# Performance work log

Hardware: AMD Instinct MI355X
Metric: run time of the kernel (lower is better)

Reference implementation:

```python
import jax, jax.numpy as jnp
import numpy as np

B, S, HID = 2, 2048, 2048
H, HKV, D = 16, 8, 128
CHUNK = 512
THETA = 1000000.0
NEG = -1e9


def setup_inputs() -> dict:
    key = jax.random.key(0)
    ks = jax.random.split(key, 10)
    hidden_states = jax.random.normal(ks[0], (B, S, HID), dtype=jnp.float32)
    # additive causal mask (0 on/below diagonal, -1e9 above)
    tri = jnp.tril(jnp.ones((S, S), dtype=bool))
    attention_mask = jnp.where(tri, 0.0, NEG).astype(jnp.float32)
    attention_mask = jnp.broadcast_to(attention_mask[None, None], (B, 1, S, S))
    w = 0.02
    Wq = jax.random.normal(ks[1], (HID, H * D), dtype=jnp.float32) * w
    bq = jax.random.normal(ks[2], (H * D,), dtype=jnp.float32) * w
    Wk = jax.random.normal(ks[3], (HID, HKV * D), dtype=jnp.float32) * w
    bk = jax.random.normal(ks[4], (HKV * D,), dtype=jnp.float32) * w
    Wv = jax.random.normal(ks[5], (HID, HKV * D), dtype=jnp.float32) * w
    bv = jax.random.normal(ks[6], (HKV * D,), dtype=jnp.float32) * w
    Wo = jax.random.normal(ks[7], (H * D, HID), dtype=jnp.float32) * w
    bo = jax.random.normal(ks[8], (HID,), dtype=jnp.float32) * w
    return {"hidden_states": hidden_states, "attention_mask": attention_mask,
            "Wq": Wq, "bq": bq, "Wk": Wk, "bk": bk, "Wv": Wv, "bv": bv,
            "Wo": Wo, "bo": bo}


def _rope_tables(seq_len, dim):
    inv_freq = 1.0 / (THETA ** (jnp.arange(0, dim, 2, dtype=jnp.float32) / dim))
    pos = jnp.arange(seq_len, dtype=jnp.float32)
    freqs = pos[:, None] * inv_freq[None, :]          # [S, D/2]
    emb = jnp.concatenate([freqs, freqs], axis=-1)    # [S, D]
    return jnp.cos(emb)[None, None], jnp.sin(emb)[None, None]  # [1,1,S,D]


def _rotate_half(x):
    x1, x2 = jnp.split(x, 2, axis=-1)
    return jnp.concatenate([-x2, x1], axis=-1)


def _attn_forward(hidden_states, attention_mask, Wq, bq, Wk, bk, Wv, bv, Wo, bo):
    bsz, s, _ = hidden_states.shape
    q = (hidden_states @ Wq + bq).reshape(bsz, s, H, D).transpose(0, 2, 1, 3)
    k = (hidden_states @ Wk + bk).reshape(bsz, s, HKV, D).transpose(0, 2, 1, 3)
    v = (hidden_states @ Wv + bv).reshape(bsz, s, HKV, D).transpose(0, 2, 1, 3)
    cos, sin = _rope_tables(s, D)
    q = q * cos + _rotate_half(q) * sin
    k = k * cos + _rotate_half(k) * sin
    n_rep = H // HKV
    k = jnp.repeat(k, n_rep, axis=1)  # repeat_kv
    v = jnp.repeat(v, n_rep, axis=1)
    scale = 1.0 / jnp.sqrt(jnp.float32(D))
    nq, nk = s // CHUNK, s // CHUNK
    Qc = q.reshape(bsz, H, nq, CHUNK, D)
    Kc = jnp.moveaxis(k.reshape(bsz, H, nk, CHUNK, D), 2, 0)   # [nk,B,H,Ck,D]
    Vc = jnp.moveaxis(v.reshape(bsz, H, nk, CHUNK, D), 2, 0)
    Mc = jnp.moveaxis(attention_mask.reshape(bsz, 1, nq, CHUNK, nk, CHUNK), 4, 0)  # [nk,B,1,nq,Cq,Ck]

    def step(carry, xs):
        o, m, d = carry
        k_seg, v_seg, m_seg = xs
        # scores: [B,H,nq,Cq,Ck]
        sc = jnp.einsum('bhqcd,bhkd->bhqck', Qc, k_seg) * scale + m_seg
        new_m = jnp.maximum(m, sc.max(axis=-1, keepdims=True))
        e = jnp.exp(sc - new_m)
        sums = e.sum(axis=-1, keepdims=True)
        prev = jnp.exp(m - new_m)          # NOTE: uses running max, as in source
        d_new = prev + sums
        o = (o * prev + jnp.einsum('bhqck,bhkd->bhqcd', e, v_seg)) / d_new
        return (o, new_m, d_new), None

    o0 = jnp.zeros((bsz, H, nq, CHUNK, D), dtype=jnp.float32)
    m0 = jnp.full((bsz, H, nq, CHUNK, 1), -jnp.inf, dtype=jnp.float32)
    d0 = jnp.ones((bsz, H, nq, CHUNK, 1), dtype=jnp.float32)
    (o, m, d), _ = jax.lax.scan(step, (o0, m0, d0), (Kc, Vc, Mc))
    # final rescale: attn_output * exp(max - logsumexp) == o / d_last (source math)
    o = o / d
    attn = o.reshape(bsz, H, s, D).transpose(0, 2, 1, 3).reshape(bsz, s, H * D)
    return attn @ Wo + bo


def reference(hidden_states, attention_mask, Wq, bq, Wk, bk, Wv, bv, Wo, bo):
    return _attn_forward(hidden_states, attention_mask, Wq, bq, Wk, bk, Wv, bv, Wo, bo)
```

## Files before the change

kernel.cpp:

```cpp
#include <hip/hip_runtime.h>
#include <hip/hip_bf16.h>


typedef __attribute__((ext_vector_type(8))) short s8v;
typedef __attribute__((ext_vector_type(4))) float f4v;
typedef __attribute__((ext_vector_type(4))) unsigned int u32x4;

#define MFMA16(a, b, c) __builtin_amdgcn_mfma_f32_16x16x32_bf16((a), (b), (c), 0, 0, 0)

typedef unsigned short u16;
typedef const __attribute__((address_space(1))) unsigned int* gas_p;
typedef __attribute__((address_space(3))) unsigned int* las_p;

template <bool B> struct BoolC { static constexpr bool value = B; };

__device__ __forceinline__ void gl_lds16(const void* g, void* l) {
    __builtin_amdgcn_global_load_lds((gas_p)g, (las_p)l, 16, 0, 0);
}

__device__ __forceinline__ u16 f2b(float f) {
    __hip_bfloat16 h = __float2bfloat16(f);
    return *reinterpret_cast<u16*>(&h);
}
__device__ __forceinline__ float b2f(u16 u) {
    __hip_bfloat16 h;
    *reinterpret_cast<u16*>(&h) = u;
    return __bfloat162float(h);
}

__device__ __forceinline__ void qswap(unsigned int& a, unsigned int& b) {
#if __has_builtin(__builtin_amdgcn_permlane32_swap) && __has_builtin(__builtin_amdgcn_permlane16_swap)
    typedef __attribute__((ext_vector_type(2))) unsigned int u32x2;
    u32x2 r1 = __builtin_amdgcn_permlane32_swap(a, b, false, false);
    u32x2 r2 = __builtin_amdgcn_permlane16_swap(r1[0], r1[1], false, false);
    a = r2[0]; b = r2[1];
#else
    asm volatile("v_permlane32_swap_b32 %0, %1\n\t"
                 "s_nop 0\n\t"
                 "v_permlane16_swap_b32 %0, %1\n\t"
                 "s_nop 0"
                 : "+v"(a), "+v"(b));
#endif
}

__device__ const unsigned char qt_tab[40] = {
    4, 5, 6, 7,
    8, 8, 9, 9, 10, 10, 11, 11,
    12, 12, 12, 13, 13, 13, 14, 14, 14, 15, 15, 15,
    3, 7, 11, 15, 2, 6, 10, 14, 1, 5, 9, 13, 0, 4, 8, 12};
__device__ const unsigned char c_tab[40] = {
    0, 0, 0, 0,
    0, 1, 0, 1, 0, 1, 0, 1,
    0, 1, 2, 0, 1, 2, 0, 1, 2, 0, 1, 2,
    0, 1, 2, 3, 0, 1, 2, 3, 0, 1, 2, 3, 0, 1, 2, 3};

__device__ __forceinline__ int uoff40(int qt, int c) {
    int qc = qt >> 2;
    if (c < qc) {
        if (qt < 8) return qt - 4;
        if (qt < 12) return 4 + ((qt - 8) << 1) + c;
        return 12 + (qt - 12) * 3 + c;
    }
    return 24 + ((3 - (qt & 3)) << 2) + qc;
}

__global__ __launch_bounds__(256) void k_cast_hs(const float* __restrict__ src,
                                                 u16* __restrict__ dst) {
    int i = blockIdx.x * 256 + threadIdx.x;
    float4 v = reinterpret_cast<const float4*>(src)[i];
    alignas(8) u16 t[4] = {f2b(v.x), f2b(v.y), f2b(v.z), f2b(v.w)};
    reinterpret_cast<uint2*>(dst)[i] = *reinterpret_cast<uint2*>(t);
}

__global__ __launch_bounds__(256) void k_transpose_w(
    const float* __restrict__ Wq, const float* __restrict__ Wk,
    const float* __restrict__ Wv, const float* __restrict__ Wo,
    u16* __restrict__ wt_all, u16* __restrict__ wo_t) {
    int id = blockIdx.x;
    const float* W; u16* dst; int N, nbase;
    if (id < 4096)      { W = Wq; dst = wt_all; N = 2048; nbase = 0; }
    else if (id < 6144) { W = Wk; dst = wt_all; N = 1024; nbase = 2048; id -= 4096; }
    else if (id < 8192) { W = Wv; dst = wt_all; N = 1024; nbase = 3072; id -= 6144; }
    else                { W = Wo; dst = wo_t;  N = 2048; nbase = 0;    id -= 8192; }
    int tiles_n = N >> 5;
    int k0 = (id / tiles_n) << 5, n0 = (id % tiles_n) << 5;
    __shared__ float t[32][33];
    int tid = threadIdx.x;
    {
        int row = tid >> 3, c4 = (tid & 7) << 2;
        float4 v = *reinterpret_cast<const float4*>(&W[(size_t)(k0 + row) * N + n0 + c4]);
        t[row][c4 + 0] = v.x; t[row][c4 + 1] = v.y;
        t[row][c4 + 2] = v.z; t[row][c4 + 3] = v.w;
    }
    __syncthreads();
    {
        int n = tid >> 3, kq = (tid & 7) << 2;
        alignas(8) u16 p[4];
#pragma unroll
        for (int j = 0; j < 4; j++) p[j] = f2b(t[kq + j][n]);
        *reinterpret_cast<uint2*>(&dst[(size_t)(nbase + n0 + n) * 2048 + k0 + kq]) =
            *reinterpret_cast<uint2*>(p);
    }
}

__global__ __launch_bounds__(256) void k_bias(const float* __restrict__ bq,
                                              const float* __restrict__ bk,
                                              const float* __restrict__ bv,
                                              float* __restrict__ dst) {
    int i = blockIdx.x * 256 + threadIdx.x;
    float v = (i < 2048) ? bq[i] : (i < 3072) ? bk[i - 2048] : bv[i - 3072];
    dst[i] = v;
}

__global__ __launch_bounds__(256) void k_gemm(
    const u16* __restrict__ A, const u16* __restrict__ Bt,
    const float* __restrict__ bias, void* __restrict__ out,
    int M, int N, int K, int out_f32) {
    __shared__ alignas(16) u16 As[2][128][64];
    __shared__ alignas(16) u16 Bs[2][128][64];
    int tid = threadIdx.x;
    int wave = tid >> 6, lane = tid & 63, quad = lane >> 4, l16 = lane & 15;
    int nwg = gridDim.x * gridDim.y;
    int wg = blockIdx.y * gridDim.x + blockIdx.x;
    int l = (wg & 7) * (nwg >> 3) + (wg >> 3);
    int t4 = l >> 4, a4 = l & 15;
    int tn4 = gridDim.x >> 2;
    int tm = t4 / tn4, tn = t4 % tn4;
    int m0 = ((tm << 2) + (a4 >> 2)) << 7;
    int n0 = ((tn << 2) + (a4 & 3)) << 7;
    int wm = (wave >> 1) << 6, wn = (wave & 1) << 6;
    f4v zero = {0.f, 0.f, 0.f, 0.f};
    f4v acc[4][4];
#pragma unroll
    for (int a = 0; a < 4; a++)
#pragma unroll
        for (int b = 0; b < 4; b++) acc[a][b] = zero;
    int r0 = tid >> 3;
    int gsw = (tid & 7) ^ (r0 & 7);
    const u16* gA = A + (size_t)(m0 + r0) * K + (gsw << 3);
    const u16* gB = Bt + (size_t)(n0 + r0) * K + (gsw << 3);
    auto stage = [&](int k0, int buf) {
#pragma unroll
        for (int i = 0; i < 4; i++) {
            gl_lds16(gA + (size_t)(i << 5) * K + k0,
                     (char*)&As[buf][0][0] + (i << 12) + tid * 16);
            gl_lds16(gB + (size_t)(i << 5) * K + k0,
                     (char*)&Bs[buf][0][0] + (i << 12) + tid * 16);
        }
    };
    int NT = K >> 6;
    stage(0, 0);
    stage(64, 1);
    for (int t = 0; t < NT; t++) {
        int cur = t & 1;
        if (t + 1 < NT)
            asm volatile("s_waitcnt vmcnt(8)" ::: "memory");
        else
            asm volatile("s_waitcnt vmcnt(0)" ::: "memory");
        __builtin_amdgcn_sched_barrier(0);
        __builtin_amdgcn_s_barrier();
        __builtin_amdgcn_sched_barrier(0);
#pragma unroll
        for (int ks = 0; ks < 2; ks++) {
            int rg = (((ks << 2) | quad) ^ (l16 & 7)) << 3;
            s8v af[4], bf_[4];
#pragma unroll
            for (int mi = 0; mi < 4; mi++)
                af[mi] = *reinterpret_cast<const s8v*>(&As[cur][wm + mi * 16 + l16][rg]);
#pragma unroll
            for (int ni = 0; ni < 4; ni++)
                bf_[ni] = *reinterpret_cast<const s8v*>(&Bs[cur][wn + ni * 16 + l16][rg]);
#pragma unroll
            for (int mi = 0; mi < 4; mi++)
#pragma unroll
                for (int ni = 0; ni < 4; ni++)
                    acc[mi][ni] = MFMA16(af[mi], bf_[ni], acc[mi][ni]);
        }
        asm volatile("s_waitcnt lgkmcnt(0)" ::: "memory");
        __builtin_amdgcn_sched_barrier(0);
        __builtin_amdgcn_s_barrier();
        __builtin_amdgcn_sched_barrier(0);
        if (t + 2 < NT) stage((t + 2) << 6, cur);
    }
    if (!out_f32) {
        u16* cs = &As[0][0][0];
#pragma unroll
        for (int ni = 0; ni < 4; ni++) {
            int col = wn + ni * 16 + l16;
            float bsv = bias[n0 + col];
#pragma unroll
            for (int mi = 0; mi < 4; mi++)
#pragma unroll
                for (int r = 0; r < 4; r++) {
                    int row = wm + mi * 16 + (quad << 2) + r;
                    cs[row * 128 + ((((col >> 3) ^ (row & 7)) << 3) | (col & 7))] =
                        f2b(acc[mi][ni][r] + bsv);
                }
        }
        __syncthreads();
        int row = tid >> 1, c8 = (tid & 1) << 3;
        u16* dst = (u16*)out + (size_t)(m0 + row) * N + n0 + (c8 << 3);
#pragma unroll
        for (int j = 0; j < 8; j++) {
            int g = (c8 + j) ^ (row & 7);
            *reinterpret_cast<uint4*>(dst + j * 8) =
                *reinterpret_cast<const uint4*>(&cs[row * 128 + g * 8]);
        }
    } else {
        float* cf = (float*)&As[0][0][0];
#pragma unroll
        for (int p = 0; p < 2; p++) {
            __syncthreads();
            if ((wm >> 6) == p) {
#pragma unroll
                for (int ni = 0; ni < 4; ni++) {
                    int col = wn + ni * 16 + l16;
                    float bsv = bias[n0 + col];
#pragma unroll
                    for (int mi = 0; mi < 4; mi++)
#pragma unroll
                        for (int r = 0; r < 4; r++) {
                            int lr = (wm - (p << 6)) + mi * 16 + (quad << 2) + r;
                            cf[lr * 128 + ((((col >> 2) ^ (lr & 7)) << 2) | (col & 3))] =
                                acc[mi][ni][r] + bsv;
                        }
                }
            }
            __syncthreads();
            int row = tid >> 2, g0 = (tid & 3) << 3;
            float* dst = (float*)out + (size_t)(m0 + (p << 6) + row) * N + n0 + (g0 << 2);
#pragma unroll
            for (int j = 0; j < 8; j++) {
                int g = (g0 + j) ^ (row & 7);
                *reinterpret_cast<uint4*>(dst + j * 4) =
                    *reinterpret_cast<const uint4*>(&cf[row * 128 + g * 4]);
            }
        }
    }
}

__global__ __launch_bounds__(256) void k_rope(const u16* __restrict__ qkv,
                                              u16* __restrict__ qr,
                                              u16* __restrict__ kr) {
    const float qscale = 0.08838834764831845f * 1.44269504088896340f;
    int row = blockIdx.x;
    int b = row >> 11, s = row & 2047;
    const u16* src = qkv + (size_t)row * 4096;
    __shared__ float lcs[64], lsn[64];
    int tid = threadIdx.x;
    if (tid < 64) {
        float fr = (float)s * exp2f((float)tid * -0.31143075889569023f);
        lcs[tid] = cosf(fr);
        lsn[tid] = sinf(fr);
    }
    __syncthreads();
    for (int u = tid; u < 1536; u += 256) {
        int hh, i;
        const u16* sp;
        u16* dp;
        float sc;
        if (u < 1024) {
            hh = u >> 6; i = u & 63;
            sp = src + hh * 128;
            dp = qr + ((size_t)(b * 16 + hh) * 2048 + s) * 128;
            sc = qscale;
        } else {
            int u2 = u - 1024;
            hh = u2 >> 6; i = u2 & 63;
            sp = src + 2048 + hh * 128;
            dp = kr + ((size_t)(b * 8 + hh) * 2048 + s) * 128;
            sc = 1.f;
        }
        float x1 = b2f(sp[i]);
        float x2 = b2f(sp[i + 64]);
        float cs = lcs[i], sn = lsn[i];
        dp[i]      = f2b((x1 * cs - x2 * sn) * sc);
        dp[i + 64] = f2b((x2 * cs + x1 * sn) * sc);
    }
}

__global__ __launch_bounds__(256) void k_vtrans(const u16* __restrict__ qkv,
                                                u16* __restrict__ vt) {
    int bkv = blockIdx.z, b = bkv >> 3, kv = bkv & 7;
    int s0 = blockIdx.x << 6, d0 = blockIdx.y << 5;
    __shared__ alignas(16) u16 t[32][72];
    int tid = threadIdx.x, c = tid & 31, rr = tid >> 5;
#pragma unroll
    for (int i = 0; i < 8; i++) {
        int s = s0 + rr + i * 8;
        t[c][rr + i * 8] = qkv[(size_t)(b * 2048 + s) * 4096 + 3072 + kv * 128 + d0 + c];
    }
    __syncthreads();
    int dd = tid >> 3, sc8 = (tid & 7) << 3;
    *reinterpret_cast<uint4*>(&vt[((size_t)(b * 8 + kv) * 128 + d0 + dd) * 2048 + s0 + sc8]) =
        *reinterpret_cast<const uint4*>(&t[dd][sc8]);
}

__global__ __launch_bounds__(256, 3) void k_attn_part(const u16* __restrict__ qr,
                                                      const u16* __restrict__ kr,
                                                      const u16* __restrict__ vt,
                                                      u16* __restrict__ PVp,
                                                      float* __restrict__ scp) {
    const float NINF = -__builtin_inff();
    __shared__ alignas(16) u16 Ks[2][64 * 128];
    __shared__ alignas(16) u16 Vs[128 * 64];

    int tid = threadIdx.x;
    int wv = tid >> 6, lane = tid & 63, quad = lane >> 4, l16 = lane & 15;
    int x = blockIdx.x, h = blockIdx.y, b = blockIdx.z, kvh = h >> 1;
    int qt = qt_tab[x], c = c_tab[x], qc = qt >> 2;
    bool diag = (c == qc);
    int m3 = qt & 3;
    int nt = diag ? ((m3 + 1) << 1) : 8;
    int kbase = c << 9;
    const u16* Qp = qr + ((size_t)(b * 16 + h) * 2048 + qt * 128 + wv * 32) * 128;
    const u16* Kp = kr + ((size_t)(b * 8 + kvh) * 2048) * 128;
    const u16* Vp = vt + ((size_t)(b * 8 + kvh) * 128) * 2048;

    s8v qf0[4], qf1[4];
#pragma unroll
    for (int sl = 0; sl < 4; sl++) {
        qf0[sl] = *reinterpret_cast<const s8v*>(&Qp[l16 * 128 + sl * 32 + (quad << 3)]);
        qf1[sl] = *reinterpret_cast<const s8v*>(&Qp[(16 + l16) * 128 + sl * 32 + (quad << 3)]);
    }
    s8v ones;
#pragma unroll
    for (int i = 0; i < 8; i++) ones[i] = (short)0x3F80;
    s8v pzero;
#pragma unroll
    for (int i = 0; i < 8; i++) pzero[i] = (short)0;

    int krow = tid >> 4, kg = (tid & 15) ^ krow;
    int vd = tid >> 3, vg = (tid & 7) ^ (vd & 7);
    auto stageK = [&](int t) {
        int kbt = kbase + (t << 6);
        const u16* kgp = Kp + (size_t)(kbt + krow) * 128 + (kg << 3);
        char* kd = (char*)&Ks[t & 1][0];
#pragma unroll
        for (int i = 0; i < 4; i++)
            gl_lds16(kgp + (size_t)(i << 4) * 128, kd + (i << 12) + tid * 16);
    };
    auto stageV = [&](int t) {
        int kbt = kbase + (t << 6);
        const u16* vgp = Vp + (size_t)vd * 2048 + kbt + (vg << 3);
        char* vdst = (char*)&Vs[0];
#pragma unroll
        for (int i = 0; i < 4; i++)
            gl_lds16(vgp + (size_t)(i << 5) * 2048, vdst + (i << 12) + tid * 16);
    };

    auto pack = [&](const f4v& s, bool tri, bool act, float& tmx,
                    unsigned int& wlo, unsigned int& whi) {
        if (!act) { wlo = 0u; whi = 0u; return; }
        float e[4];
#pragma unroll
        for (int r = 0; r < 4; r++) {
            float v = s[r];
            if (tri && ((quad << 2) + r > l16)) v = NINF;
            tmx = fmaxf(tmx, v);
            e[r] = __builtin_amdgcn_exp2f(v);
        }
        wlo = (unsigned int)f2b(e[0]) | ((unsigned int)f2b(e[1]) << 16);
        whi = (unsigned int)f2b(e[2]) | ((unsigned int)f2b(e[3]) << 16);
    };

    f4v zero = {0.f, 0.f, 0.f, 0.f};
    f4v u0[8], u1[8], sums0 = zero, sums1 = zero;
#pragma unroll
    for (int ni = 0; ni < 8; ni++) { u0[ni] = zero; u1[ni] = zero; }
    float tmx0 = NINF, tmx1 = NINF;
    int qg0 = wv << 1, qg1 = (wv << 1) + 1;

    auto run = [&](auto diagc) {
        constexpr bool DIAG = decltype(diagc)::value;
        stageK(0);
        for (int t = 0; t < nt; t++) {
            __syncthreads();
            stageV(t);
            if (t + 1 < nt) stageK(t + 1);
            const char* Kbuf = (const char*)&Ks[t & 1][0];
            int kgb = DIAG ? ((t << 2) - (m3 << 3)) : 0;
            s8v pa0s[2], pa1s[2];
            bool act0[2], act1[2];
#pragma unroll
            for (int s2 = 0; s2 < 2; s2++) {
                int kgA = kgb + (s2 << 1), kgB = kgA + 1;
                bool skip = DIAG && (kgA > qg1);
                bool a0 = !DIAG || (kgA <= qg0);
                bool b0 = !DIAG || (kgB <= qg0);
                bool b1 = !DIAG || (kgB <= qg1);
                act1[s2] = !skip;
                act0[s2] = !skip && a0;
                if (skip) { pa0s[s2] = pzero; pa1s[s2] = pzero; continue; }
                f4v sA0 = zero, sA1 = zero, sB0 = zero, sB1 = zero;
#pragma unroll
                for (int sl = 0; sl < 4; sl++) {
                    s8v kf = *reinterpret_cast<const s8v*>(
                        Kbuf + (((s2 << 1) << 4) + l16) * 256 +
                        ((((sl << 2) + quad) ^ l16) << 4));
                    if (a0) sA0 = MFMA16(kf, qf0[sl], sA0);
                    sA1 = MFMA16(kf, qf1[sl], sA1);
                }
                if (b1) {
#pragma unroll
                    for (int sl = 0; sl < 4; sl++) {
                        s8v kf = *reinterpret_cast<const s8v*>(
                            Kbuf + ((((s2 << 1) | 1) << 4) + l16) * 256 +
                            ((((sl << 2) + quad) ^ l16) << 4));
                        if (b0) sB0 = MFMA16(kf, qf0[sl], sB0);
                        sB1 = MFMA16(kf, qf1[sl], sB1);
                    }
                }
                unsigned int A0w, A1w, B0w, B1w;
                pack(sA1, DIAG && (kgA == qg1), true, tmx1, A0w, A1w);
                pack(sB1, DIAG && (kgB == qg1), b1, tmx1, B0w, B1w);
                qswap(A0w, B0w); qswap(A1w, B1w);
                u32x4 pw1 = {A0w, A1w, B0w, B1w};
                pa1s[s2] = __builtin_bit_cast(s8v, pw1);
                if (a0) {
                    unsigned int C0w, C1w, D0w, D1w;
                    pack(sA0, DIAG && (kgA == qg0), true, tmx0, C0w, C1w);
                    pack(sB0, DIAG && (kgB == qg0), b0, tmx0, D0w, D1w);
                    qswap(C0w, D0w); qswap(C1w, D1w);
                    u32x4 pw0 = {C0w, C1w, D0w, D1w};
                    pa0s[s2] = __builtin_bit_cast(s8v, pw0);
                } else {
                    pa0s[s2] = pa1s[s2];
                }
            }
            __syncthreads();
#pragma unroll
            for (int s2 = 0; s2 < 2; s2++) {
                if (DIAG && !act1[s2]) continue;
                bool a0 = !DIAG || act0[s2];
                if (a0) sums0 = MFMA16(pa0s[s2], ones, sums0);
                sums1 = MFMA16(pa1s[s2], ones, sums1);
#pragma unroll
                for (int ni = 0; ni < 8; ni++) {
                    s8v vf = *reinterpret_cast<const s8v*>(
                        (const char*)&Vs[0] + ((ni << 4) + l16) * 128 +
                        ((((s2 << 2) + quad) ^ (l16 & 7)) << 4));
                    if (a0) u0[ni] = MFMA16(pa0s[s2], vf, u0[ni]);
                    u1[ni] = MFMA16(pa1s[s2], vf, u1[ni]);
                }
            }
        }
    };
    if (diag) run(BoolC<true>{}); else run(BoolC<false>{});

    tmx0 = fmaxf(tmx0, __shfl_xor(tmx0, 16));
    tmx0 = fmaxf(tmx0, __shfl_xor(tmx0, 32));
    tmx1 = fmaxf(tmx1, __shfl_xor(tmx1, 16));
    tmx1 = fmaxf(tmx1, __shfl_xor(tmx1, 32));
    float m0[4], m1[4], resc0[4], resc1[4];
#pragma unroll
    for (int r = 0; r < 4; r++) {
        m0[r] = __shfl(tmx0, (quad << 2) + r);
        m1[r] = __shfl(tmx1, (quad << 2) + r);
        resc0[r] = __builtin_amdgcn_exp2f(-m0[r]);
        resc1[r] = __builtin_amdgcn_exp2f(-m1[r]);
    }
    int slot = (b * 16 + h) * 40 + x;
    u16* pvdst = PVp + (size_t)slot * 16384;
    int row0 = wv * 32 + (quad << 2);
#pragma unroll
    for (int ni = 0; ni < 8; ni++)
#pragma unroll
        for (int r = 0; r < 4; r++) {
            pvdst[(row0 + r) * 128 + ni * 16 + l16] = f2b(u0[ni][r] * resc0[r]);
            pvdst[(row0 + 16 + r) * 128 + ni * 16 + l16] = f2b(u1[ni][r] * resc1[r]);
        }
    if (l16 == 0) {
        float* scd = scp + (size_t)slot * 256 + row0;
#pragma unroll
        for (int r = 0; r < 4; r++) {
            scd[r] = m0[r] * 0.6931471805599453f;
            scd[16 + r] = m1[r] * 0.6931471805599453f;
            scd[128 + r] = sums0[r] * resc0[r];
            scd[144 + r] = sums1[r] * resc1[r];
        }
    }
}

__global__ __launch_bounds__(256) void k_attn_comb(const u16* __restrict__ PVp,
                                                   const float* __restrict__ scp,
                                                   u16* __restrict__ attnb) {
    int qt64 = blockIdx.x, h = blockIdx.y, b = blockIdx.z;
    int qt = qt64 >> 1, qc = qt >> 2;
    int tid = threadIdx.x;
    int row = ((qt64 & 1) << 6) + (tid >> 2), d0 = (tid & 3) << 5;
    int bh = b * 16 + h;
    float o[32];
#pragma unroll
    for (int i = 0; i < 32; i++) o[i] = 0.f;
    float mprev = -__builtin_inff(), dlast = 1.f;
    for (int cc = 0; cc <= qc; cc++) {
        int slot = bh * 40 + uoff40(qt, cc);
        float ch = scp[(size_t)slot * 256 + row];
        float sh = scp[(size_t)slot * 256 + 128 + row];
        float mnew = fmaxf(mprev, ch);
        float p = __expf(mprev - mnew);
        float lam = __expf(ch - mnew);
        float dd = p + lam * sh;
        float inv = 1.f / dd;
        const u16* pv = PVp + (size_t)slot * 16384 + row * 128 + d0;
#pragma unroll
        for (int k = 0; k < 4; k++) {
            s8v v8 = *reinterpret_cast<const s8v*>(pv + (k << 3));
#pragma unroll
            for (int j = 0; j < 8; j++) {
                int i = (k << 3) + j;
                o[i] = (o[i] * p + lam * b2f((u16)v8[j])) * inv;
            }
        }
        mprev = mnew;
        dlast = dd;
    }
    if (qc == 3) {
        float inv = 1.f / dlast;
#pragma unroll
        for (int i = 0; i < 32; i++) o[i] *= inv;
    }
    alignas(16) u16 ob[32];
#pragma unroll
    for (int i = 0; i < 32; i++) ob[i] = f2b(o[i]);
    u16* dst = attnb + (size_t)(b * 2048 + qt * 128 + row) * 2048 + h * 128 + d0;
#pragma unroll
    for (int k = 0; k < 4; k++)
        reinterpret_cast<uint4*>(dst)[k] = reinterpret_cast<const uint4*>(ob)[k];
}

extern "C" void kernel_launch(void* const* d_in, const int* in_sizes, int n_in,
                              void* d_out, int out_size, void* d_ws, size_t ws_size,
                              hipStream_t stream) {
    (void)in_sizes; (void)n_in; (void)out_size; (void)ws_size;
    const float* hs = (const float*)d_in[0];
    const float* Wq = (const float*)d_in[2];
    const float* bq = (const float*)d_in[3];
    const float* Wk = (const float*)d_in[4];
    const float* bk = (const float*)d_in[5];
    const float* Wv = (const float*)d_in[6];
    const float* bv = (const float*)d_in[7];
    const float* Wo = (const float*)d_in[8];
    const float* bo = (const float*)d_in[9];

    char* ws = (char*)d_ws;
    u16* hsb      = (u16*)(ws);
    u16* qr       = hsb;
    u16* attnb    = hsb;
    u16* wt_all   = (u16*)(ws + (16u << 20));
    u16* kr       = wt_all;
    u16* vt       = (u16*)(ws + (24u << 20));
    u16* wo_t     = (u16*)(ws + (32u << 20));
    float* bias_c = (float*)(ws + (40u << 20));
    u16* qkv      = (u16*)(ws + (40u << 20) + 65536);
    u16* PVp      = qkv;
    float* scp    = (float*)(ws + (40u << 20) + 65536 + 41943040u);

    k_cast_hs<<<8192, 256, 0, stream>>>(hs, hsb);
    k_transpose_w<<<12288, 256, 0, stream>>>(Wq, Wk, Wv, Wo, wt_all, wo_t);
    k_bias<<<16, 256, 0, stream>>>(bq, bk, bv, bias_c);
    k_gemm<<<dim3(32, 32), 256, 0, stream>>>(hsb, wt_all, bias_c, qkv,
                                             4096, 4096, 2048, 0);
    k_rope<<<4096, 256, 0, stream>>>(qkv, qr, kr);
    k_vtrans<<<dim3(32, 4, 16), 256, 0, stream>>>(qkv, vt);
    k_attn_part<<<dim3(40, 16, 2), 256, 0, stream>>>(qr, kr, vt, PVp, scp);
    k_attn_comb<<<dim3(32, 16, 2), 256, 0, stream>>>(PVp, scp, attnb);
    k_gemm<<<dim3(16, 32), 256, 0, stream>>>(attnb, wo_t, bo, d_out,
                                             4096, 2048, 2048, 1);
}
```

Measured before the change: 377.7 us.

## Use 256x256-tile 512-thread GEMM for fused QKV projection

Adds a new bf16 MFMA GEMM kernel with 256x256 output tiles, 8 waves each computing 128x64, and a staggered A/B double-buffer pipeline using direct global-to-LDS loads with swizzling. It replaces the 128x128 GEMM for the QKV projection, cutting global/LDS traffic per FLOP through larger tile reuse. The grid drops to 256 workgroups on a 256-CU part, exactly one wave of blocks, and the larger accumulator footprint (128 fp32 per lane) raises register pressure. The epilogue writes bf16 with scattered stride-N stores.

```diff
diff --git a/kernel.cpp b/kernel.cpp
--- a/kernel.cpp
+++ b/kernel.cpp
@@ -110,6 +110,109 @@
     int i = blockIdx.x * 256 + threadIdx.x;
     float v = (i < 2048) ? bq[i] : (i < 3072) ? bk[i - 2048] : bv[i - 3072];
     dst[i] = v;
+}
+
+__global__ __launch_bounds__(512) void k_gemm256(
+    const u16* __restrict__ A, const u16* __restrict__ Bt,
+    const float* __restrict__ bias, u16* __restrict__ out,
+    int M, int N, int K) {
+    __shared__ alignas(16) u16 As[2][256][64];
+    __shared__ alignas(16) u16 Bs[2][256][64];
+    int tid = threadIdx.x;
+    int wave = tid >> 6, lane = tid & 63, quad = lane >> 4, l16 = lane & 15;
+    int gx = gridDim.x;
+    int nb = gx * gridDim.y;
+    int wg = blockIdx.y * gx + blockIdx.x;
+    int lsw = (wg & 7) * (nb >> 3) + (wg >> 3);
+    int tm = lsw / gx, tn = lsw % gx;
+    int m0 = tm << 8, n0 = tn << 8;
+    int wm = (wave >> 2) << 7;
+    int wn = (wave & 3) << 6;
+    f4v zero = {0.f, 0.f, 0.f, 0.f};
+    f4v acc[8][4];
+#pragma unroll
+    for (int a = 0; a < 8; a++)
+#pragma unroll
+        for (int b = 0; b < 4; b++) acc[a][b] = zero;
+    int sr = tid >> 3, sg = (tid & 7) ^ (sr & 7);
+    const u16* gA = A + (size_t)(m0 + sr) * K + (sg << 3);
+    const u16* gB = Bt + (size_t)(n0 + sr) * K + (sg << 3);
+    auto stageA = [&](int t) {
+        char* d = (char*)&As[t & 1][0][0];
+        int k0 = t << 6;
+#pragma unroll
+        for (int j = 0; j < 4; j++)
+            gl_lds16(gA + (size_t)(j << 6) * K + k0, d + (j << 13) + tid * 16);
+    };
+    auto stageB = [&](int t) {
+        char* d = (char*)&Bs[t & 1][0][0];
+        int k0 = t << 6;
+#pragma unroll
+        for (int j = 0; j < 4; j++)
+            gl_lds16(gB + (size_t)(j << 6) * K + k0, d + (j << 13) + tid * 16);
+    };
+    int NT = K >> 6;
+    stageA(0); stageB(0); stageB(1);
+    for (int t = 0; t < NT; t++) {
+        int cur = t & 1;
+        if (t + 1 < NT)
+            asm volatile("s_waitcnt vmcnt(4)" ::: "memory");
+        else
+            asm volatile("s_waitcnt vmcnt(0)" ::: "memory");
+        __builtin_amdgcn_sched_barrier(0);
+        __builtin_amdgcn_s_barrier();
+        __builtin_amdgcn_sched_barrier(0);
+        if (t + 1 < NT) stageA(t + 1);
+        s8v bf[2][4], af[8];
+#pragma unroll
+        for (int kk = 0; kk < 2; kk++)
+#pragma unroll
+            for (int ni = 0; ni < 4; ni++)
+                bf[kk][ni] = *reinterpret_cast<const s8v*>(
+                    &Bs[cur][wn + ni * 16 + l16][((((kk << 2) | quad) ^ (l16 & 7)) << 3)]);
+#pragma unroll
+        for (int mi = 0; mi < 8; mi++)
+            af[mi] = *reinterpret_cast<const s8v*>(
+                &As[cur][wm + mi * 16 + l16][((quad ^ (l16 & 7)) << 3)]);
+        asm volatile("s_waitcnt lgkmcnt(0)" ::: "memory");
+        __builtin_amdgcn_sched_barrier(0);
+        __builtin_amdgcn_s_setprio(1);
+#pragma unroll
+        for (int mi = 0; mi < 8; mi++)
+#pragma unroll
+            for (int ni = 0; ni < 4; ni++)
+                acc[mi][ni] = MFMA16(af[mi], bf[0][ni], acc[mi][ni]);
+        __builtin_amdgcn_s_setprio(0);
+        __builtin_amdgcn_sched_barrier(0);
+        __builtin_amdgcn_s_barrier();
+        __builtin_amdgcn_sched_barrier(0);
+        if (t + 2 < NT) stageB(t + 2);
+#pragma unroll
+        for (int mi = 0; mi < 8; mi++)
+            af[mi] = *reinterpret_cast<const s8v*>(
+                &As[cur][wm + mi * 16 + l16][(((4 | quad) ^ (l16 & 7)) << 3)]);
+        asm volatile("s_waitcnt lgkmcnt(0)" ::: "memory");
+        __builtin_amdgcn_sched_barrier(0);
+        __builtin_amdgcn_s_setprio(1);
+#pragma unroll
+        for (int mi = 0; mi < 8; mi++)
+#pragma unroll
+            for (int ni = 0; ni < 4; ni++)
+                acc[mi][ni] = MFMA16(af[mi], bf[1][ni], acc[mi][ni]);
+        __builtin_amdgcn_s_setprio(0);
+        __builtin_amdgcn_sched_barrier(0);
+    }
+#pragma unroll
+    for (int ni = 0; ni < 4; ni++) {
+        int n = n0 + wn + ni * 16 + l16;
+        float bsv = bias[n];
+#pragma unroll
+        for (int mi = 0; mi < 8; mi++)
+#pragma unroll
+            for (int r = 0; r < 4; r++)
+                out[(size_t)(m0 + wm + mi * 16 + (quad << 2) + r) * N + n] =
+                    f2b(acc[mi][ni][r] + bsv);
+    }
 }
 
 __global__ __launch_bounds__(256) void k_gemm(
@@ -560,8 +663,8 @@
     k_cast_hs<<<8192, 256, 0, stream>>>(hs, hsb);
     k_transpose_w<<<12288, 256, 0, stream>>>(Wq, Wk, Wv, Wo, wt_all, wo_t);
     k_bias<<<16, 256, 0, stream>>>(bq, bk, bv, bias_c);
-    k_gemm<<<dim3(32, 32), 256, 0, stream>>>(hsb, wt_all, bias_c, qkv,
-                                             4096, 4096, 2048, 0);
+    k_gemm256<<<dim3(16, 16), 512, 0, stream>>>(hsb, wt_all, bias_c, qkv,
+                                                4096, 4096, 2048);
     k_rope<<<4096, 256, 0, stream>>>(qkv, qr, kr);
     k_vtrans<<<dim3(32, 4, 16), 256, 0, stream>>>(qkv, vt);
     k_attn_part<<<dim3(40, 16, 2), 256, 0, stream>>>(qr, kr, vt, PVp, scp);
```

Result: faster. 356.0 us (-5.7%).
